# Optimization experiments

Hardware: AMD Instinct MI355X
Metric: run time of the kernel (lower is better)

The kernel has to match this reference:

```python
import jax, jax.numpy as jnp
import numpy as np

B, S, D_IN, D_OUT, NUM_LAYERS = 128, 64, 2048, 2048, 64

def setup_inputs() -> dict:
    key = jax.random.key(0)
    k1, k2, k3 = jax.random.split(key, 3)
    x = jax.random.normal(k1, (B, S, D_IN), dtype=jnp.float32)
    weight = jax.random.normal(k2, (NUM_LAYERS, D_OUT, D_IN), dtype=jnp.float32)
    layer_idx = jax.random.randint(k3, (S,), 0, NUM_LAYERS, dtype=jnp.int32)
    return {"x": x, "weight": weight, "layer_idx": layer_idx}

def reference(x, weight, layer_idx):
    # x: [B, S, D_in]; weight: [L, D_out, D_in]; layer_idx: [S] ints in [0, L)
    # Per position s: out[:, s, :] = x[:, s, :] @ weight[layer_idx[s]].T
    w_sel = weight[layer_idx]                      # [S, D_out, D_in] gather
    out = jnp.einsum('bsd,sod->bso', x, w_sel)     # batched per-position GEMMs
    return out
```

## Files before the change

kernel.cpp:

```cpp
#include <hip/hip_runtime.h>
#include <hip/hip_bf16.h>

#define B_DIM 128
#define S_DIM 64
#define DIN   2048
#define DOUT  2048
#define NLAYERS 64

#define BM 128
#define BN 64
#define BK 64
#define NK (DIN / BK)
#define TPP (DOUT / BN)
#define NTILES (S_DIM * TPP)
#define NXCD 8
#define APAD 16384

typedef __bf16 bf16_t;
typedef __attribute__((ext_vector_type(8))) bf16_t bf16x8;
typedef __attribute__((ext_vector_type(4))) float f32x4;

__global__ void rank_sort(const int* __restrict__ layer_idx, int* __restrict__ tilemap) {
    __shared__ int L[S_DIM];
    const int s = threadIdx.x;
    L[s] = layer_idx[s];
    __syncthreads();
    const int mine = L[s];
    int rank = 0, gstart = 0, gcount = 0;
    #pragma unroll
    for (int t = 0; t < S_DIM; ++t) {
        const int lt = L[t];
        rank   += (lt < mine || (lt == mine && t < s)) ? 1 : 0;
        gstart += (lt <  mine) ? 1 : 0;
        gcount += (lt == mine) ? 1 : 0;
    }
    const int gpos = rank - gstart;
    for (int nb = 0; nb < TPP; ++nb)
        tilemap[gstart * TPP + nb * gcount + gpos] = (s << 5) | nb;
}

__global__ void convert_x(const float* __restrict__ x, bf16_t* __restrict__ x16) {
    const size_t i = ((size_t)blockIdx.x * 256 + threadIdx.x) * 8;
    f32x4 a = *(const f32x4*)(x + i);
    f32x4 b = *(const f32x4*)(x + i + 4);
    bf16x8 v;
    #pragma unroll
    for (int j = 0; j < 4; ++j) { v[j] = (bf16_t)a[j]; v[j + 4] = (bf16_t)b[j]; }
    *(bf16x8*)(x16 + i) = v;
}

template <bool XBF16>
__launch_bounds__(256, 2)
__global__ void flex_linear_gemm(const float* __restrict__ x,
                                 const bf16_t* __restrict__ x16,
                                 const float* __restrict__ w,
                                 const int* __restrict__ layer_idx,
                                 const int* __restrict__ tilemap,
                                 float* __restrict__ out) {
    __shared__ bf16_t Alds[BM * BK + APAD];
    __shared__ bf16_t Blds[BN * BK];

    const int orig = blockIdx.x;
    const int xcd  = orig & (NXCD - 1);
    const int slot = orig >> 3;
    const int val  = tilemap[xcd * (NTILES / NXCD) + slot];
    const int s    = val >> 5;
    const int nb   = val & 31;
    const int layer = layer_idx[s];

    const float* Bg = w + (size_t)layer * (size_t)(DOUT * DIN) + (size_t)(nb * BN) * DIN;

    const int tid  = threadIdx.x;
    const int lane = tid & 63;
    const int wave = tid >> 6;
    const int wr = (wave >> 1) * 64;
    const int wc = (wave & 1) * 32;
    const int lrow = lane & 15;
    const int lk   = (lane >> 4) * 8;

    int offWA[4], offWB[2];
    const float*  pA[4];
    const bf16_t* pA16[4];
    const float*  pB[2];
    #pragma unroll
    for (int i = 0; i < 4; ++i) {
        const int c   = tid + 256 * i;
        const int row = c >> 3;
        const int kc8 = (c & 7) * 8;
        offWA[i] = (row * BK + kc8) ^ ((row & 7) << 3);
        const size_t aoff = (size_t)row * (S_DIM * DIN) + (size_t)s * DIN + kc8;
        pA[i]   = x   + aoff;
        pA16[i] = x16 + aoff;
    }
    #pragma unroll
    for (int i = 0; i < 2; ++i) {
        const int c   = tid + 256 * i;
        const int row = c >> 3;
        const int kc8 = (c & 7) * 8;
        offWB[i] = (row * BK + kc8) ^ ((row & 7) << 3);
        pB[i] = Bg + (size_t)row * DIN + kc8;
    }
    int offA[2][4], offB[2][2];
    #pragma unroll
    for (int kk = 0; kk < 2; ++kk) {
        #pragma unroll
        for (int m = 0; m < 4; ++m) {
            const int ra = wr + m * 16 + lrow;
            offA[kk][m] = (ra * BK + kk * 32 + lk) ^ ((ra & 7) << 3);
        }
        #pragma unroll
        for (int n = 0; n < 2; ++n) {
            const int rb = wc + n * 16 + lrow;
            offB[kk][n] = (rb * BK + kk * 32 + lk) ^ ((rb & 7) << 3);
        }
    }

    bf16x8 RA16[4];
    f32x4  RA[8];
    f32x4  RB[4];
    f32x4  acc[4][2] = {};

    auto issue = [&](int kb) {
        const int koff = kb * BK;
        #pragma unroll
        for (int i = 0; i < 4; ++i) {
            if constexpr (XBF16) {
                RA16[i] = *(const bf16x8*)(pA16[i] + koff);
            } else {
                const float* a = pA[i] + koff;
                RA[2 * i]     = *(const f32x4*)a;
                RA[2 * i + 1] = *(const f32x4*)(a + 4);
            }
        }
        #pragma unroll
        for (int i = 0; i < 2; ++i) {
            const float* b = pB[i] + koff;
            RB[2 * i]     = *(const f32x4*)b;
            RB[2 * i + 1] = *(const f32x4*)(b + 4);
        }
    };
    auto cvt_write = [&]() {
        #pragma unroll
        for (int i = 0; i < 4; ++i) {
            if constexpr (XBF16) {
                *(bf16x8*)&Alds[offWA[i]] = RA16[i];
            } else {
                bf16x8 va;
                #pragma unroll
                for (int j = 0; j < 4; ++j) {
                    va[j]     = (bf16_t)RA[2 * i][j];
                    va[j + 4] = (bf16_t)RA[2 * i + 1][j];
                }
                *(bf16x8*)&Alds[offWA[i]] = va;
            }
        }
        #pragma unroll
        for (int i = 0; i < 2; ++i) {
            bf16x8 vb;
            #pragma unroll
            for (int j = 0; j < 4; ++j) {
                vb[j]     = (bf16_t)RB[2 * i][j];
                vb[j + 4] = (bf16_t)RB[2 * i + 1][j];
            }
            *(bf16x8*)&Blds[offWB[i]] = vb;
        }
    };
    auto compute = [&]() {
        #pragma unroll
        for (int kk = 0; kk < 2; ++kk) {
            bf16x8 af[4], bfr[2];
            #pragma unroll
            for (int m = 0; m < 4; ++m) af[m]  = *(const bf16x8*)&Alds[offA[kk][m]];
            #pragma unroll
            for (int n = 0; n < 2; ++n) bfr[n] = *(const bf16x8*)&Blds[offB[kk][n]];
            #pragma unroll
            for (int m = 0; m < 4; ++m)
                #pragma unroll
                for (int n = 0; n < 2; ++n)
                    acc[m][n] = __builtin_amdgcn_mfma_f32_16x16x32_bf16(af[m], bfr[n], acc[m][n], 0, 0, 0);
        }
    };

    issue(0);
    cvt_write();
    for (int kb = 0; kb < NK - 1; ++kb) {
        __syncthreads();
        issue(kb + 1);
        compute();
        __syncthreads();
        cvt_write();
    }
    __syncthreads();
    compute();

    float* Og = out + (size_t)s * DOUT + (size_t)(nb * BN);
    #pragma unroll
    for (int m = 0; m < 4; ++m) {
        const int rb = wr + m * 16 + (lane >> 4) * 4;
        #pragma unroll
        for (int r = 0; r < 4; ++r) {
            float* orow = Og + (size_t)(rb + r) * (S_DIM * DOUT);
            #pragma unroll
            for (int n = 0; n < 2; ++n)
                __builtin_nontemporal_store(acc[m][n][r], &orow[wc + n * 16 + (lane & 15)]);
        }
    }
}

extern "C" void kernel_launch(void* const* d_in, const int* in_sizes, int n_in,
                              void* d_out, int out_size, void* d_ws, size_t ws_size,
                              hipStream_t stream) {
    const float* x         = (const float*)d_in[0];
    const float* w         = (const float*)d_in[1];
    const int*   layer_idx = (const int*)d_in[2];
    float*       out       = (float*)d_out;

    int*    tilemap = (int*)d_ws;
    bf16_t* x16     = (bf16_t*)((char*)d_ws + 16384);
    const size_t need = 16384 + (size_t)B_DIM * S_DIM * DIN * sizeof(bf16_t);

    rank_sort<<<1, S_DIM, 0, stream>>>(layer_idx, tilemap);

    if (ws_size >= need) {
        convert_x<<<(B_DIM * S_DIM * DIN / 8) / 256, 256, 0, stream>>>(x, x16);
        flex_linear_gemm<true><<<NTILES, dim3(256), 0, stream>>>(x, x16, w, layer_idx, tilemap, out);
    } else {
        flex_linear_gemm<false><<<NTILES, dim3(256), 0, stream>>>(x, x16, w, layer_idx, tilemap, out);
    }
}
```

Before: 224.0 us.

## Pair same-layer positions per block to reuse weight tiles across two GEMMs

```diff
diff --git a/kernel.cpp b/kernel.cpp
--- a/kernel.cpp
+++ b/kernel.cpp
@@ -14,29 +14,51 @@
 #define TPP (DOUT / BN)
 #define NTILES (S_DIM * TPP)
 #define NXCD 8
-#define APAD 16384
+
+#define A0_OFF 0
+#define A1_OFF (BM * BK)
+#define B_OFF  (2 * BM * BK)
+#define LDS_ELEMS (2 * BM * BK + BN * BK + 8192)
 
 typedef __bf16 bf16_t;
 typedef __attribute__((ext_vector_type(8))) bf16_t bf16x8;
 typedef __attribute__((ext_vector_type(4))) float f32x4;
 
 __global__ void rank_sort(const int* __restrict__ layer_idx, int* __restrict__ tilemap) {
-    __shared__ int L[S_DIM];
+    __shared__ int L[S_DIM], gposA[S_DIM];
+    __shared__ int chunkWork[S_DIM];
     const int s = threadIdx.x;
     L[s] = layer_idx[s];
     __syncthreads();
     const int mine = L[s];
-    int rank = 0, gstart = 0, gcount = 0;
-    #pragma unroll
+    int rank = 0, gstart = 0;
     for (int t = 0; t < S_DIM; ++t) {
         const int lt = L[t];
         rank   += (lt < mine || (lt == mine && t < s)) ? 1 : 0;
         gstart += (lt <  mine) ? 1 : 0;
-        gcount += (lt == mine) ? 1 : 0;
     }
     const int gpos = rank - gstart;
-    for (int nb = 0; nb < TPP; ++nb)
-        tilemap[gstart * TPP + nb * gcount + gpos] = (s << 5) | nb;
+    gposA[s] = gpos;
+    __syncthreads();
+    const bool prim = (gpos & 1) == 0;
+    int cidx = 0, partner = -1;
+    for (int t = 0; t < S_DIM; ++t) {
+        if (((gposA[t] & 1) == 0) && (L[t] < mine || (L[t] == mine && gposA[t] < gpos))) cidx++;
+        if (L[t] == mine && gposA[t] == gpos + 1) partner = t;
+    }
+    if (prim) chunkWork[cidx] = (partner >= 0) ? 2 : 1;
+    for (int i = 0; i < NTILES / S_DIM; ++i) tilemap[s * (NTILES / S_DIM) + i] = -1;
+    __syncthreads();
+    if (prim) {
+        int cum = 0;
+        for (int j = 0; j < cidx; ++j) cum += chunkWork[j];
+        const int xcd = cum >> 3;
+        int off = 0, c2 = 0;
+        for (int j = 0; j < cidx; ++j) { if ((c2 >> 3) == xcd) off++; c2 += chunkWork[j]; }
+        const int base = xcd * (NTILES / NXCD) + off * TPP;
+        const int code = (s << 5) | ((partner + 1) << 11);
+        for (int nb = 0; nb < TPP; ++nb) tilemap[base + nb] = code | nb;
+    }
 }
 
 __global__ void convert_x(const float* __restrict__ x, bf16_t* __restrict__ x16) {
@@ -57,16 +79,16 @@
                                  const int* __restrict__ layer_idx,
                                  const int* __restrict__ tilemap,
                                  float* __restrict__ out) {
-    __shared__ bf16_t Alds[BM * BK + APAD];
-    __shared__ bf16_t Blds[BN * BK];
-
-    const int orig = blockIdx.x;
-    const int xcd  = orig & (NXCD - 1);
-    const int slot = orig >> 3;
-    const int val  = tilemap[xcd * (NTILES / NXCD) + slot];
-    const int s    = val >> 5;
-    const int nb   = val & 31;
-    const int layer = layer_idx[s];
+    __shared__ bf16_t lds[LDS_ELEMS];
+
+    const int e = tilemap[blockIdx.x];
+    if (e < 0) return;
+    const int nb   = e & 31;
+    const int s0   = (e >> 5) & 63;
+    const int s1p1 = (e >> 11) & 127;
+    const bool has2 = s1p1 > 0;
+    const int s1   = has2 ? (s1p1 - 1) : s0;
+    const int layer = layer_idx[s0];
 
     const float* Bg = w + (size_t)layer * (size_t)(DOUT * DIN) + (size_t)(nb * BN) * DIN;
 
@@ -79,8 +101,8 @@
     const int lk   = (lane >> 4) * 8;
 
     int offWA[4], offWB[2];
-    const float*  pA[4];
-    const bf16_t* pA16[4];
+    const float*  pA0[4], *pA1[4];
+    const bf16_t* pA016[4], *pA116[4];
     const float*  pB[2];
     #pragma unroll
     for (int i = 0; i < 4; ++i) {
@@ -88,9 +110,11 @@
         const int row = c >> 3;
         const int kc8 = (c & 7) * 8;
         offWA[i] = (row * BK + kc8) ^ ((row & 7) << 3);
-        const size_t aoff = (size_t)row * (S_DIM * DIN) + (size_t)s * DIN + kc8;
-        pA[i]   = x   + aoff;
-        pA16[i] = x16 + aoff;
+        const size_t base = (size_t)row * (S_DIM * DIN) + kc8;
+        pA0[i]   = x   + base + (size_t)s0 * DIN;
+        pA016[i] = x16 + base + (size_t)s0 * DIN;
+        pA1[i]   = x   + base + (size_t)s1 * DIN;
+        pA116[i] = x16 + base + (size_t)s1 * DIN;
     }
     #pragma unroll
     for (int i = 0; i < 2; ++i) {
@@ -115,21 +139,33 @@
         }
     }
 
-    bf16x8 RA16[4];
-    f32x4  RA[8];
+    bf16x8 RA0[4], RA1[4];
+    f32x4  RAF0[8], RAF1[8];
     f32x4  RB[4];
-    f32x4  acc[4][2] = {};
+    f32x4  acc0[4][2] = {}, acc1[4][2] = {};
 
     auto issue = [&](int kb) {
         const int koff = kb * BK;
         #pragma unroll
         for (int i = 0; i < 4; ++i) {
             if constexpr (XBF16) {
-                RA16[i] = *(const bf16x8*)(pA16[i] + koff);
+                RA0[i] = *(const bf16x8*)(pA016[i] + koff);
             } else {
-                const float* a = pA[i] + koff;
-                RA[2 * i]     = *(const f32x4*)a;
-                RA[2 * i + 1] = *(const f32x4*)(a + 4);
+                const float* a = pA0[i] + koff;
+                RAF0[2 * i]     = *(const f32x4*)a;
+                RAF0[2 * i + 1] = *(const f32x4*)(a + 4);
+            }
+        }
+        if (has2) {
+            #pragma unroll
+            for (int i = 0; i < 4; ++i) {
+                if constexpr (XBF16) {
+                    RA1[i] = *(const bf16x8*)(pA116[i] + koff);
+                } else {
+                    const float* a = pA1[i] + koff;
+                    RAF1[2 * i]     = *(const f32x4*)a;
+                    RAF1[2 * i + 1] = *(const f32x4*)(a + 4);
+                }
             }
         }
         #pragma unroll
@@ -143,15 +179,31 @@
         #pragma unroll
         for (int i = 0; i < 4; ++i) {
             if constexpr (XBF16) {
-                *(bf16x8*)&Alds[offWA[i]] = RA16[i];
+                *(bf16x8*)&lds[A0_OFF + offWA[i]] = RA0[i];
             } else {
                 bf16x8 va;
                 #pragma unroll
                 for (int j = 0; j < 4; ++j) {
-                    va[j]     = (bf16_t)RA[2 * i][j];
-                    va[j + 4] = (bf16_t)RA[2 * i + 1][j];
-                }
-                *(bf16x8*)&Alds[offWA[i]] = va;
+                    va[j]     = (bf16_t)RAF0[2 * i][j];
+                    va[j + 4] = (bf16_t)RAF0[2 * i + 1][j];
+                }
+                *(bf16x8*)&lds[A0_OFF + offWA[i]] = va;
+            }
+        }
+        if (has2) {
+            #pragma unroll
+            for (int i = 0; i < 4; ++i) {
+                if constexpr (XBF16) {
+                    *(bf16x8*)&lds[A1_OFF + offWA[i]] = RA1[i];
+                } else {
+                    bf16x8 va;
+                    #pragma unroll
+                    for (int j = 0; j < 4; ++j) {
+                        va[j]     = (bf16_t)RAF1[2 * i][j];
+                        va[j + 4] = (bf16_t)RAF1[2 * i + 1][j];
+                    }
+                    *(bf16x8*)&lds[A1_OFF + offWA[i]] = va;
+                }
             }
         }
         #pragma unroll
@@ -162,22 +214,31 @@
                 vb[j]     = (bf16_t)RB[2 * i][j];
                 vb[j + 4] = (bf16_t)RB[2 * i + 1][j];
             }
-            *(bf16x8*)&Blds[offWB[i]] = vb;
+            *(bf16x8*)&lds[B_OFF + offWB[i]] = vb;
         }
     };
     auto compute = [&]() {
         #pragma unroll
         for (int kk = 0; kk < 2; ++kk) {
-            bf16x8 af[4], bfr[2];
-            #pragma unroll
-            for (int m = 0; m < 4; ++m) af[m]  = *(const bf16x8*)&Alds[offA[kk][m]];
-            #pragma unroll
-            for (int n = 0; n < 2; ++n) bfr[n] = *(const bf16x8*)&Blds[offB[kk][n]];
-            #pragma unroll
-            for (int m = 0; m < 4; ++m)
+            bf16x8 bfr[2];
+            #pragma unroll
+            for (int n = 0; n < 2; ++n) bfr[n] = *(const bf16x8*)&lds[B_OFF + offB[kk][n]];
+            #pragma unroll
+            for (int m = 0; m < 4; ++m) {
+                bf16x8 af = *(const bf16x8*)&lds[A0_OFF + offA[kk][m]];
                 #pragma unroll
                 for (int n = 0; n < 2; ++n)
-                    acc[m][n] = __builtin_amdgcn_mfma_f32_16x16x32_bf16(af[m], bfr[n], acc[m][n], 0, 0, 0);
+                    acc0[m][n] = __builtin_amdgcn_mfma_f32_16x16x32_bf16(af, bfr[n], acc0[m][n], 0, 0, 0);
+            }
+            if (has2) {
+                #pragma unroll
+                for (int m = 0; m < 4; ++m) {
+                    bf16x8 af = *(const bf16x8*)&lds[A1_OFF + offA[kk][m]];
+                    #pragma unroll
+                    for (int n = 0; n < 2; ++n)
+                        acc1[m][n] = __builtin_amdgcn_mfma_f32_16x16x32_bf16(af, bfr[n], acc1[m][n], 0, 0, 0);
+                }
+            }
         }
     };
 
@@ -193,18 +254,22 @@
     __syncthreads();
     compute();
 
-    float* Og = out + (size_t)s * DOUT + (size_t)(nb * BN);
-    #pragma unroll
-    for (int m = 0; m < 4; ++m) {
-        const int rb = wr + m * 16 + (lane >> 4) * 4;
-        #pragma unroll
-        for (int r = 0; r < 4; ++r) {
-            float* orow = Og + (size_t)(rb + r) * (S_DIM * DOUT);
-            #pragma unroll
-            for (int n = 0; n < 2; ++n)
-                __builtin_nontemporal_store(acc[m][n][r], &orow[wc + n * 16 + (lane & 15)]);
-        }
-    }
+    auto store_pos = [&](int sp, f32x4 (&ac)[4][2]) {
+        float* Og = out + (size_t)sp * DOUT + (size_t)(nb * BN);
+        #pragma unroll
+        for (int m = 0; m < 4; ++m) {
+            const int rb = wr + m * 16 + (lane >> 4) * 4;
+            #pragma unroll
+            for (int r = 0; r < 4; ++r) {
+                float* orow = Og + (size_t)(rb + r) * (S_DIM * DOUT);
+                #pragma unroll
+                for (int n = 0; n < 2; ++n)
+                    __builtin_nontemporal_store(ac[m][n][r], &orow[wc + n * 16 + (lane & 15)]);
+            }
+        }
+    };
+    store_pos(s0, acc0);
+    if (has2) store_pos(s1, acc1);
 }
 
 extern "C" void kernel_launch(void* const* d_in, const int* in_sizes, int n_in,
```

New measurement: 222.9 us. No clear change (-0.5%).
